# Performance work log

Measured on AMD Instinct MI355X. Metric: run time of the kernel, lower is better.

## Reference

```python
import jax, jax.numpy as jnp
import numpy as np

B, WS, DIM, HEADS, AGENT, PS = 128, 14, 256, 8, 49, 7
N = WS * WS


def conv(x, w, b, pad, groups=1):
    y = jax.lax.conv_general_dilated(x, w, (1, 1), [(pad, pad), (pad, pad)],
                                     dimension_numbers=('NCHW', 'OIHW', 'NCHW'),
                                     feature_group_count=groups)
    return y + b[None, :, None, None]


def bilinear_resize(x, oh, ow):
    # F.interpolate(mode='bilinear', align_corners=False) on last two dims
    ih, iw = x.shape[-2], x.shape[-1]
    def grid(ni, no):
        pos = np.maximum((np.arange(no) + 0.5) * (ni / no) - 0.5, 0.0)
        i0 = np.minimum(np.floor(pos).astype(np.int32), ni - 1)
        i1 = np.minimum(i0 + 1, ni - 1)
        return i0, i1, (pos - i0).astype(np.float32)
    i0h, i1h, lh = grid(ih, oh)
    i0w, i1w, lw = grid(iw, ow)
    xh = x[..., i0h, :] * (1.0 - lh)[:, None] + x[..., i1h, :] * lh[:, None]
    return xh[..., i0w] * (1.0 - lw) + xh[..., i1w] * lw


def rel_pos_index(h, w):
    coords = np.stack(np.meshgrid(np.arange(h), np.arange(w), indexing='ij')).reshape(2, -1)
    rel = (coords[:, :, None] - coords[:, None, :]).transpose(1, 2, 0).copy()
    rel[..., 0] += h - 1
    rel[..., 1] += w - 1
    rel[..., 0] *= 2 * w - 1
    return rel.sum(-1)  # (h*w, h*w)


def cbam(x, caa1_w, caa1_b, caa2_w, caa2_b, cam1_w, cam1_b, cam2_w, cam2_b, sa_w, sa_b):
    # ChannelAttention: both conv stacks act on 1x1 pooled maps -> only kernel centers matter
    avgp = x.mean((2, 3))
    t1 = jax.nn.relu(jnp.einsum('oi,bi->bo', caa1_w[:, :, 1, 1], avgp) + caa1_b)
    y1 = jax.nn.sigmoid(jnp.einsum('oi,bi->bo', caa2_w[:, :, 1, 1], t1) + caa2_b)
    mxp = x.max((2, 3))
    t2 = jax.nn.relu(jnp.einsum('oi,bi->bo', cam1_w[:, :, 0, 0], mxp) + cam1_b)
    y2 = jax.nn.sigmoid(jnp.einsum('oi,bi->bo', cam2_w[:, :, 0, 0], t2) + cam2_b)
    x = jax.nn.sigmoid(y1 + y2)[:, :, None, None] * x
    # Spatial attention
    mask = jnp.concatenate([x.mean(1, keepdims=True), x.max(1, keepdims=True)], axis=1)
    mask = jax.nn.sigmoid(conv(mask, sa_w, sa_b, 4))
    return x * mask


def chan_inter(x, ci1_w, ci1_b, bn_g, bn_b, ci2_w, ci2_b):
    # AdaptiveAvgPool2d(1) then 5x5 convs on 1x1 maps -> kernel-center matmuls; BN in eval mode
    p = x.mean((2, 3))
    t = jnp.einsum('oi,bi->bo', ci1_w[:, :, 2, 2], p) + ci1_b
    t = jax.nn.relu(bn_g * t * (1.0 / np.sqrt(1.0 + 1e-5)) + bn_b)
    return jnp.einsum('oi,bi->bo', ci2_w[:, :, 2, 2], t) + ci2_b


def setup_inputs() -> dict:
    key = jax.random.key(0)
    ks = jax.random.split(key, 40)
    d, r = DIM, DIM // 16
    p = lambda i, shape, s=0.02: jax.random.normal(ks[i], shape, jnp.float32) * s
    return {
        'x': jax.random.normal(ks[0], (B, N, d), jnp.float32),
        'h': WS,
        'w': WS,
        'lka_w': p(1, (3 * d, 1, 5, 5)), 'lka_b': p(2, (3 * d,)),
        'conv5_w': p(3, (d, d, 5, 5)), 'conv5_b': p(4, (d,)),
        'caa1_w': p(5, (r, d, 3, 3)), 'caa1_b': p(6, (r,)),
        'caa2_w': p(7, (d, r, 3, 3)), 'caa2_b': p(8, (d,)),
        'cam1_w': p(9, (r, d, 1, 1)), 'cam1_b': p(10, (r,)),
        'cam2_w': p(11, (d, r, 1, 1)), 'cam2_b': p(12, (d,)),
        'sa_w': p(13, (1, 2, 9, 9)), 'sa_b': p(14, (1,)),
        'ci1_w': p(15, (r, d, 5, 5)), 'ci1_b': p(16, (r,)),
        'bn_g': jnp.ones((r,), jnp.float32), 'bn_b': jnp.zeros((r,), jnp.float32),
        'ci2_w': p(17, (d, r, 5, 5)), 'ci2_b': p(18, (d,)),
        'rpb_table': p(19, ((2 * WS - 1) * (2 * WS - 1), HEADS)),
        'an_bias': p(20, (HEADS, AGENT, 7, 7)), 'na_bias': p(21, (HEADS, AGENT, 7, 7)),
        'ah_bias': p(22, (1, HEADS, AGENT, WS, 1)), 'aw_bias': p(23, (1, HEADS, AGENT, 1, WS)),
        'ha_bias': p(24, (1, HEADS, WS, 1, AGENT)), 'wa_bias': p(25, (1, HEADS, 1, WS, AGENT)),
        'dwc_w': p(26, (d, 1, 5, 5)), 'dwc_b': p(27, (d,)),
        'proj_w': p(28, (d, d)), 'proj_b': p(29, (d,)),
    }


def reference(x, h, w, lka_w, lka_b, conv5_w, conv5_b, caa1_w, caa1_b, caa2_w, caa2_b,
              cam1_w, cam1_b, cam2_w, cam2_b, sa_w, sa_b, ci1_w, ci1_b, bn_g, bn_b,
              ci2_w, ci2_b, rpb_table, an_bias, na_bias, ah_bias, aw_bias, ha_bias,
              wa_bias, dwc_w, dwc_b, proj_w, proj_b):
    b, n, c = x.shape
    heads, agent, ps = HEADS, AGENT, PS
    hd = c // heads
    scale = hd ** (-0.5)

    xc = jnp.transpose(x.reshape(b, h, w, c), (0, 3, 1, 2))  # (b,c,h,w)
    y = conv(xc, lka_w, lka_b, 2, groups=c)                   # depthwise, 3 outputs/group
    k_raw, v_raw, q_raw = y[:, :c], y[:, c:2 * c], y[:, 2 * c:]

    # v branch: conv5 then raw reshape-scramble (faithful to torch .reshape of NCHW), then CBAM
    v5 = jnp.transpose(conv(v_raw, conv5_w, conv5_b, 2).reshape(b, h, w, c), (0, 3, 1, 2))
    vc = cbam(v5, caa1_w, caa1_b, caa2_w, caa2_b, cam1_w, cam1_b, cam2_w, cam2_b, sa_w, sa_b)
    v_feat = jnp.transpose(vc.reshape(b, c, n), (0, 2, 1))    # (b,n,c)

    # adaptive avg/max pool 14->7 == exact 2x2 pooling
    at = q_raw.reshape(b, c, ps, h // ps, ps, w // ps).mean((3, 5)).reshape(b, c, agent).transpose(0, 2, 1)
    atk = k_raw.reshape(b, c, ps, h // ps, ps, w // ps).max((3, 5)).reshape(b, c, agent).transpose(0, 2, 1)

    # raw row-major reshapes of (b,c,h,w) into (b,n,heads,hd): faithful to torch
    q = q_raw.reshape(b, n, heads, hd).transpose(0, 2, 1, 3) * scale
    k = k_raw.reshape(b, n, heads, hd).transpose(0, 2, 1, 3)
    v = v_raw.reshape(b, n, heads, hd).transpose(0, 2, 1, 3)
    v1 = v_feat.reshape(b, n, heads, hd).transpose(0, 2, 1, 3)

    # full window attention with relative position bias
    idx = rel_pos_index(h, w)
    rpb = rpb_table[idx.reshape(-1)].reshape(n, n, heads).transpose(2, 0, 1)
    attn = jax.nn.softmax(jnp.einsum('bhid,bhjd->bhij', q, k) + rpb[None])
    x1 = jnp.einsum('bhij,bhjd->bhid', attn, v).transpose(0, 2, 1, 3).reshape(b, n, c)

    ar = x1.transpose(0, 2, 1).reshape(b, c, h, w)
    cmap = chan_inter(ar, ci1_w, ci1_b, bn_g, bn_b, ci2_w, ci2_b)  # (b,c)
    conv_x2 = jax.nn.sigmoid(cmap)[:, :, None, None] * jnp.transpose(q.reshape(b, h, w, c), (0, 3, 1, 2))

    # agent attention
    at_h = at.reshape(b, agent, heads, hd).transpose(0, 2, 1, 3)
    atk_h = atk.reshape(b, agent, heads, hd).transpose(0, 2, 1, 3)
    pb = bilinear_resize(an_bias, h, w).reshape(1, heads, agent, n) \
         + (ah_bias + aw_bias).reshape(1, heads, agent, n)
    agent_attn = jax.nn.softmax(jnp.einsum('bhad,bhnd->bhan', at_h * scale, k) + pb)
    agent_attn1 = jax.nn.softmax(jnp.einsum('bhad,bhnd->bhan', atk_h * scale, q) + pb)
    agent_v = jnp.einsum('bhan,bhnd->bhad', agent_attn, v1) + jnp.einsum('bhan,bhnd->bhad', agent_attn1, v)

    ab = bilinear_resize(na_bias, h, w).reshape(1, heads, agent, n).transpose(0, 1, 3, 2) \
         + (ha_bias + wa_bias).reshape(1, heads, n, agent)
    q_attn = jax.nn.softmax(jnp.einsum('bhnd,bhad->bhna', q * scale, at_h) + ab)
    k_attn = jax.nn.softmax(jnp.einsum('bhnd,bhad->bhna', k * scale, atk_h) + ab)
    xo = jnp.einsum('bhna,bhad->bhnd', q_attn + k_attn, agent_v).transpose(0, 2, 1, 3).reshape(b, n, c)

    xo = xo + jnp.transpose(conv(conv_x2, dwc_w, dwc_b, 2, groups=c), (0, 2, 3, 1)).reshape(b, n, c)
    qc = jnp.transpose(q.transpose(0, 2, 1, 3).reshape(b, h, w, c), (0, 3, 1, 2))
    xo = xo + jnp.transpose(conv(qc, dwc_w, dwc_b, 2, groups=c), (0, 2, 3, 1)).reshape(b, n, c)

    return xo @ proj_w.T + proj_b
```

## Files before the change

kernel.cpp:

```cpp
#include <hip/hip_runtime.h>

#define NB    128
#define NC    256
#define NPOS  196
#define NHEAD 8
#define NAG   49
#define YSTR  150528
#define VOFF  50176
#define QOFF  100352
#define SCL   0.17677669529663687f

#define WS_Y    0u
#define WS_V5   19267584u
#define WS_AT   25690112u
#define WS_ATK  27295744u
#define WS_CHG  28901376u
#define WS_CMAP 28934144u
#define WS_PBT  28966912u
#define WS_AB   29043744u
#define WS_X1S  29120576u
#define WS_AGV  29153344u
#define WS_XO   30758976u
#define WS_WT   37181504u
#define WS_CWT  37247040u

typedef __attribute__((ext_vector_type(8))) _Float16 half8;
typedef __attribute__((ext_vector_type(8))) short short8;
typedef __attribute__((ext_vector_type(4))) short short4v;
typedef __attribute__((ext_vector_type(4))) float f32x4;
typedef unsigned short ushort_t;
typedef unsigned int uint_t;

__device__ __forceinline__ float sigmoidf_(float x){ return 1.0f/(1.0f+__expf(-x)); }

__device__ __forceinline__ ushort_t f2h(float x){
  _Float16 h = (_Float16)x; return __builtin_bit_cast(ushort_t, h);
}
__device__ __forceinline__ float h2f(ushort_t u){
  return (float)__builtin_bit_cast(_Float16, u);
}

__device__ __forceinline__ float bilin7(const float* __restrict__ src, int i, int j){
  float pi = fmaxf(0.5f*(float)i - 0.25f, 0.f);
  int i0 = (int)pi; if (i0 > 6) i0 = 6;
  int i1 = i0 + 1;  if (i1 > 6) i1 = 6;
  float li = pi - (float)i0;
  float pj = fmaxf(0.5f*(float)j - 0.25f, 0.f);
  int j0 = (int)pj; if (j0 > 6) j0 = 6;
  int j1 = j0 + 1;  if (j1 > 6) j1 = 6;
  float lj = pj - (float)j0;
  float v00 = src[i0*7+j0], v01 = src[i0*7+j1];
  float v10 = src[i1*7+j0], v11 = src[i1*7+j1];
  float t0 = v00*(1.f-lj) + v01*lj;
  float t1 = v10*(1.f-lj) + v11*lj;
  return t0*(1.f-li) + t1*li;
}

__device__ __forceinline__ void conv5x5_row(const float* __restrict__ plane, int r,
                                            const float* __restrict__ w25, float* acc14){
  #pragma unroll
  for (int di = 0; di < 5; ++di){
    const float4* pr = (const float4*)(plane + (r+di)*20);
    float4 p0 = pr[0], p1 = pr[1], p2 = pr[2], p3 = pr[3], p4 = pr[4];
    float row[20] = {p0.x,p0.y,p0.z,p0.w, p1.x,p1.y,p1.z,p1.w, p2.x,p2.y,p2.z,p2.w,
                     p3.x,p3.y,p3.z,p3.w, p4.x,p4.y,p4.z,p4.w};
    #pragma unroll
    for (int dj = 0; dj < 5; ++dj){
      float w = w25[di*5+dj];
      #pragma unroll
      for (int j = 0; j < 14; ++j) acc14[j] = fmaf(row[j+dj], w, acc14[j]);
    }
  }
}

__global__ void k_pbab(const float* __restrict__ an, const float* __restrict__ ah,
                       const float* __restrict__ aw, const float* __restrict__ na,
                       const float* __restrict__ ha, const float* __restrict__ wa,
                       float* __restrict__ PBT, float* __restrict__ AB){
  int bid = blockIdx.x;
  int which = (bid >= 301);
  int t = (which ? bid - 301 : bid)*256 + threadIdx.x;
  if (t >= NHEAD*NPOS*NAG) return;
  int a = t % NAG;
  int r = t / NAG;
  int n = r % NPOS;
  int h = r / NPOS;
  int i = n/14, j = n - (n/14)*14;
  if (!which){
    float v = bilin7(an + ((size_t)h*NAG + a)*49, i, j);
    v += ah[((size_t)h*NAG + a)*14 + i] + aw[((size_t)h*NAG + a)*14 + j];
    PBT[t] = v;
  } else {
    float v = bilin7(na + ((size_t)h*NAG + a)*49, i, j);
    v += ha[((size_t)h*14 + i)*NAG + a] + wa[((size_t)h*14 + j)*NAG + a];
    AB[t] = v;
  }
}

__global__ void k_wprep(const float* __restrict__ cw, ushort_t* __restrict__ Wh,
                        const float* __restrict__ pw, float* __restrict__ WT){
  int bid = blockIdx.x;
  if (bid < 800){
    int base = (bid*256 + threadIdx.x)*8;
    int r   = base >> 8;
    int co  = r & 255;
    int tap = r >> 8;
    int ci0 = base & 255;
    const float* srcb = cw + (size_t)co*6400 + (size_t)ci0*25 + tap;
    short8 o;
    #pragma unroll
    for (int e = 0; e < 8; ++e) o[e] = (short)f2h(srcb[e*25]);
    *(short8*)(Wh + base) = o;
  } else {
    int t = (bid - 800)*256 + threadIdx.x;
    int k = t >> 8, c = t & 255;
    WT[t] = pw[c*256 + k];
  }
}

__global__ __launch_bounds__(256) void k_lka(const float* __restrict__ x, const float* __restrict__ lw,
                                             const float* __restrict__ lb, float* __restrict__ Y){
  int b = blockIdx.x >> 3, gb = blockIdx.x & 7;
  int g0 = gb*32;
  __shared__ __align__(16) float pl[32*360];
  int tid = threadIdx.x;
  for (int t = tid; t < 32*360; t += 256) pl[t] = 0.f;
  __syncthreads();
  for (int t = tid; t < 32*196; t += 256){
    int gl = t & 31, s = t >> 5;
    int i = s/14, j = s - i*14;
    pl[gl*360 + (i+2)*20 + j + 2] = x[((size_t)b*196 + s)*256 + g0 + gl];
  }
  __syncthreads();
  for (int t = tid; t < 96*14; t += 256){
    int ocl = t/14, r = t - ocl*14;
    int o  = g0*3 + ocl;
    int gl = ocl/3;
    float w25[25];
    #pragma unroll
    for (int u = 0; u < 25; ++u) w25[u] = lw[o*25 + u];
    float acc[14];
    float bv = lb[o];
    #pragma unroll
    for (int j = 0; j < 14; ++j) acc[j] = bv;
    conv5x5_row(&pl[gl*360], r, w25, acc);
    float* dst = Y + ((size_t)b*768 + o)*196 + r*14;
    #pragma unroll
    for (int j = 0; j < 14; ++j) dst[j] = acc[j];
  }
}

__global__ __launch_bounds__(256, 2) void k_conv5(const float* __restrict__ Y,
    const ushort_t* __restrict__ Wh, const float* __restrict__ cb, float* __restrict__ V5){
  int b = blockIdx.x >> 2, cog = blockIdx.x & 3;
  int co0 = cog*64;
  __shared__ __align__(16) ushort_t Pt[360*40];
  __shared__ __align__(16) ushort_t Wsm[2*5*64*40];
  float* T = (float*)Wsm;
  int tid  = threadIdx.x;
  int lane = tid & 63, wv = tid >> 6;
  int mrow = lane & 15, quad = lane >> 4;

  for (int t = tid; t < 7200; t += 256) ((uint_t*)Pt)[t] = 0;

  int prow[4];
  #pragma unroll
  for (int mt = 0; mt < 4; ++mt){
    int s = wv*64 + mt*16 + mrow;
    int p0 = 0;
    if (s < 196){ int i = s/14, j = s - i*14; p0 = i*20 + j; }
    prow[mt] = p0;
  }

  f32x4 acc[4][4];
  #pragma unroll
  for (int mt = 0; mt < 4; ++mt)
    #pragma unroll
    for (int nt = 0; nt < 4; ++nt) acc[mt][nt] = (f32x4){0.f,0.f,0.f,0.f};

  const float* src = Y + (size_t)b*YSTR + VOFF;
  int wco = tid >> 2, wpart = tid & 3;
  const ushort_t* wbase = Wh + ((size_t)(co0 + wco))*256 + wpart*8;

  short8 wreg[5];
  #pragma unroll
  for (int tp = 0; tp < 5; ++tp)
    wreg[tp] = *(const short8*)(wbase + (size_t)tp*65536);

  #pragma unroll 1
  for (int cc = 0; cc < 8; ++cc){
    __syncthreads();
    for (int t = tid; t < 784; t += 256){
      int pos = t >> 2, ch = t & 3;
      int i = pos/14, j = pos - i*14;
      int p = (i+2)*20 + j + 2;
      const float* s0 = src + (size_t)(cc*32 + ch*8)*196 + pos;
      short8 pk;
      #pragma unroll
      for (int e = 0; e < 4; ++e){
        float v0 = s0[(2*e)*196];
        float v1 = s0[(2*e+1)*196];
        pk[2*e]   = (short)f2h(v0);
        pk[2*e+1] = (short)f2h(v1);
      }
      *(short8*)&Pt[p*40 + ch*8] = pk;
    }
    #pragma unroll 1
    for (int di = 0; di < 5; ++di){
      int u = cc*5 + di;
      ushort_t* wbuf = Wsm + (u & 1)*12800;
      #pragma unroll
      for (int tp = 0; tp < 5; ++tp)
        *(short8*)&wbuf[(tp*64 + wco)*40 + wpart*8] = wreg[tp];
      if (u < 39){
        int di1 = di + 1, cc1 = cc;
        if (di1 == 5){ di1 = 0; ++cc1; }
        #pragma unroll
        for (int tp = 0; tp < 5; ++tp)
          wreg[tp] = *(const short8*)(wbase + (size_t)(di1*5 + tp)*65536 + cc1*32);
      }
      __syncthreads();
      #pragma unroll
      for (int dj = 0; dj < 5; ++dj){
        half8 a[4], bb[4];
        #pragma unroll
        for (int nt = 0; nt < 4; ++nt){
          int co = nt*16 + mrow;
          bb[nt] = *(const half8*)&wbuf[(dj*64 + co)*40 + quad*8];
        }
        #pragma unroll
        for (int mt = 0; mt < 4; ++mt){
          int p = prow[mt] + di*20 + dj;
          a[mt] = *(const half8*)&Pt[p*40 + quad*8];
        }
        #pragma unroll
        for (int mt = 0; mt < 4; ++mt)
          #pragma unroll
          for (int nt = 0; nt < 4; ++nt)
            acc[mt][nt] = __builtin_amdgcn_mfma_f32_16x16x32_f16(a[mt], bb[nt], acc[mt][nt], 0, 0, 0);
      }
    }
  }

  #pragma unroll
  for (int hf = 0; hf < 2; ++hf){
    __syncthreads();
    #pragma unroll
    for (int ntl = 0; ntl < 2; ++ntl){
      int nt = hf*2 + ntl;
      int col = ntl*16 + mrow;
      #pragma unroll
      for (int mt = 0; mt < 4; ++mt){
        int sbase = wv*64 + mt*16 + quad*4;
        #pragma unroll
        for (int r = 0; r < 4; ++r){
          int s = sbase + r;
          if (s < 196) T[col*200 + s] = acc[mt][nt][r];
        }
      }
    }
    __syncthreads();
    for (int t = tid; t < 6272; t += 256){
      int cl = t / 196;
      int f = (co0 + hf*32)*196 + t;
      float val = T[t + cl*4] + cb[co0 + hf*32 + cl];
      V5[(size_t)b*50176 + (size_t)(f & 255)*196 + (f >> 8)] = val;
    }
  }
}

__global__ __launch_bounds__(256) void k_pool(const float* __restrict__ Y, float* __restrict__ AT, float* __restrict__ ATK){
  int b = blockIdx.x >> 1, half = blockIdx.x & 1;
  int c = (threadIdx.x & 127) + half*128;
  int a0 = (threadIdx.x >> 7) ? 25 : 0;
  int a1 = (threadIdx.x >> 7) ? 49 : 25;
  const float* qp = Y + ((size_t)b*768 + 512 + c)*196;
  const float* kp = Y + ((size_t)b*768 + c)*196;
  for (int a = a0; a < a1; ++a){
    int p1 = a/7, p2 = a - p1*7;
    int s = p1*28 + p2*2;
    float q0 = qp[s], q1 = qp[s+1], q2 = qp[s+14], q3 = qp[s+15];
    AT[((size_t)b*49 + a)*256 + c] = 0.25f*(q0+q1+q2+q3);
    float k0 = kp[s], k1 = kp[s+1], k2 = kp[s+14], k3 = kp[s+15];
    ATK[((size_t)b*49 + a)*256 + c] = fmaxf(fmaxf(k0,k1), fmaxf(k2,k3));
  }
}

__global__ __launch_bounds__(256) void k_cbam(float* __restrict__ V5,
    const float* __restrict__ caa1w, const float* __restrict__ caa1b,
    const float* __restrict__ caa2w, const float* __restrict__ caa2b,
    const float* __restrict__ cam1w, const float* __restrict__ cam1b,
    const float* __restrict__ cam2w, const float* __restrict__ cam2b,
    const float* __restrict__ saw, const float* __restrict__ sab){
  int b = blockIdx.x;
  __shared__ float avg[256], mx[256], t1[16], t2[16], chg[256];
  __shared__ float mp[22*22], xp[22*22];
  __shared__ float mk[196];
  int tid = threadIdx.x, wv = tid >> 6, lane = tid & 63;
  float* v5b = V5 + (size_t)b*50176;

  for (int t = tid; t < 484; t += 256){ mp[t] = 0.f; xp[t] = 0.f; }

  for (int c = wv; c < 256; c += 4){
    float s, m;
    if (lane < 49){
      float4 v = *(const float4*)(v5b + c*196 + lane*4);
      s = v.x + v.y + v.z + v.w;
      m = fmaxf(fmaxf(v.x, v.y), fmaxf(v.z, v.w));
    } else { s = 0.f; m = -1e30f; }
    #pragma unroll
    for (int off = 1; off < 64; off <<= 1){
      s += __shfl_xor(s, off);
      m = fmaxf(m, __shfl_xor(m, off));
    }
    if (lane == 0){ avg[c] = s*(1.0f/196.0f); mx[c] = m; }
  }
  __syncthreads();

  if (tid < 16){
    float a1 = caa1b[tid], a2 = cam1b[tid];
    #pragma unroll 4
    for (int k = 0; k < 256; ++k){
      a1 = fmaf(caa1w[(tid*256 + k)*9 + 4], avg[k], a1);
      a2 = fmaf(cam1w[tid*256 + k], mx[k], a2);
    }
    t1[tid] = fmaxf(a1, 0.f);
    t2[tid] = fmaxf(a2, 0.f);
  }
  __syncthreads();
  {
    float y1 = caa2b[tid], y2 = cam2b[tid];
    #pragma unroll
    for (int k = 0; k < 16; ++k){
      y1 = fmaf(caa2w[(tid*16 + k)*9 + 4], t1[k], y1);
      y2 = fmaf(cam2w[tid*16 + k], t2[k], y2);
    }
    chg[tid] = sigmoidf_(sigmoidf_(y1) + sigmoidf_(y2));
  }
  __syncthreads();

  if (tid < 196){
    int i = tid/14, j = tid - i*14;
    float s = 0.f, m = -1e30f;
    const float* vb = v5b + tid;
    for (int c = 0; c < 256; ++c){
      float v = chg[c] * vb[c*196];
      s += v; m = fmaxf(m, v);
    }
    mp[(i+4)*22 + j+4] = s*(1.f/256.f);
    xp[(i+4)*22 + j+4] = m;
  }
  __syncthreads();
  if (tid < 196){
    int i = tid/14, j = tid - i*14;
    float acc = sab[0];
    for (int di = 0; di < 9; ++di){
      #pragma unroll
      for (int dj = 0; dj < 9; ++dj){
        acc = fmaf(mp[(i+di)*22 + j+dj], saw[di*9+dj], acc);
        acc = fmaf(xp[(i+di)*22 + j+dj], saw[81 + di*9+dj], acc);
      }
    }
    mk[tid] = sigmoidf_(acc);
  }
  __syncthreads();
  if (tid < 196){
    float m = mk[tid];
    float* vb = v5b + tid;
    for (int c = 0; c < 256; ++c) vb[c*196] = chg[c]*vb[c*196]*m;
  }
}

__global__ __launch_bounds__(512, 4) void k_attn3(const float* __restrict__ Y,
    const float* __restrict__ rpbt, float* __restrict__ X1S){
  int b = blockIdx.x >> 3, h = blockIdx.x & 7;
  __shared__ __align__(16) ushort_t Qh[208*32];
  __shared__ __align__(16) ushort_t Kh[208*32];
  __shared__ __align__(16) ushort_t E[80*208];
  __shared__ float rp[736];
  __shared__ int   rpo[208];
  __shared__ float pl2[80][2];
  __shared__ float invl[80];
  __shared__ float wj[208];
  __shared__ float wpart[8][208];
  __shared__ float xpart[16][32];
  int tid = threadIdx.x, wv = tid >> 6, lane = tid & 63;
  int mrow = lane & 15, quad = lane >> 4;
  int sw8 = ((quad ^ ((mrow >> 1) & 3)) << 3);
  const float* yb = Y + (size_t)b*YSTR;

  for (int t = tid; t < 736; t += 512) rp[t] = (t < 729) ? rpbt[t*8 + h] : 0.f;
  for (int j = tid; j < 208; j += 512){
    int jc = (j < 196) ? j : 195;
    int rj = jc/14;
    rpo[j] = rj*27 + (jc - rj*14);
    wj[j] = 0.f;
  }
  for (int t = tid; t < 384; t += 512){
    int arr = t >= 192; int u = t - arr*192;
    ((uint_t*)(arr ? Kh : Qh))[3136 + u] = 0;
  }
  for (int t = tid; t < 3136; t += 512){
    int n = t >> 4, w = t & 15;
    int ws = (((w >> 2) ^ ((n >> 1) & 3)) << 2) | (w & 3);
    const float2 qv = *(const float2*)(yb + QOFF + (size_t)n*256 + h*32 + (w << 1));
    ((uint_t*)Qh)[n*16 + ws] = (uint_t)f2h(qv.x*SCL) | ((uint_t)f2h(qv.y*SCL) << 16);
    const float2 kv = *(const float2*)(yb + (size_t)n*256 + h*32 + (w << 1));
    ((uint_t*)Kh)[n*16 + ws] = (uint_t)f2h(kv.x) | ((uint_t)f2h(kv.y) << 16);
  }
  __syncthreads();

  int mt0 = (wv & 1) ? 7 : 0;
  int mt1 = (wv & 1) ? 13 : 7;

  #pragma unroll 1
  for (int seg = 0; seg < 3; ++seg){
    int base = (seg == 0) ? 0 : (seg == 1) ? 80 : 144;
    int ntl  = (seg == 0) ? 5 : 4;
    int segrows = ntl*16;
    int vrows = 196 - base; if (vrows > segrows) vrows = segrows;

    #pragma unroll 1
    for (int ncl = (wv >> 1); ncl < ntl; ncl += 4){
      int n = base + ncl*16 + mrow;
      half8 bfr = *(const half8*)&Qh[n*32 + sw8];
      int nclamp = (n < 196) ? n : 195;
      int rin = nclamp/14, cin = nclamp - rin*14;
      int bidxn = (rin + 13)*27 + (cin + 13);
      float lsum = 0.f;
      #pragma unroll 1
      for (int mt = mt0; mt < mt1; ++mt){
        half8 afr = *(const half8*)&Kh[(mt*16 + mrow)*32 + sw8];
        f32x4 c = (f32x4){0.f,0.f,0.f,0.f};
        c = __builtin_amdgcn_mfma_f32_16x16x32_f16(afr, bfr, c, 0, 0, 0);
        int j0 = mt*16 + quad*4;
        int4 ro = *(const int4*)&rpo[j0];
        short4v pk;
        #pragma unroll
        for (int r = 0; r < 4; ++r){
          int j = j0 + r;
          int roff = (r == 0) ? ro.x : (r == 1) ? ro.y : (r == 2) ? ro.z : ro.w;
          float e = (j < 196) ? __expf(c[r] + rp[bidxn - roff]) : 0.f;
          lsum += e;
          pk[r] = (short)f2h(e);
        }
        if (n < 196) *(short4v*)&E[(n - base)*208 + j0] = pk;
      }
      lsum += __shfl_xor(lsum, 16);
      lsum += __shfl_xor(lsum, 32);
      if (quad == 0) pl2[n - base][wv & 1] = lsum;
    }
    __syncthreads();
    for (int t = tid; t < vrows; t += 512) invl[t] = 1.f/(pl2[t][0] + pl2[t][1]);
    __syncthreads();

    {
      int j0 = lane*4;
      if (j0 < 208){
        float a0=0.f,a1=0.f,a2=0.f,a3=0.f;
        #pragma unroll 1
        for (int nl = wv; nl < vrows; nl += 8){
          float iv = invl[nl];
          short4v ev = *(const short4v*)&E[nl*208 + j0];
          a0 = fmaf(h2f((ushort_t)ev[0]), iv, a0);
          a1 = fmaf(h2f((ushort_t)ev[1]), iv, a1);
          a2 = fmaf(h2f((ushort_t)ev[2]), iv, a2);
          a3 = fmaf(h2f((ushort_t)ev[3]), iv, a3);
        }
        *(f32x4*)&wpart[wv][j0] = (f32x4){a0,a1,a2,a3};
      }
    }
    __syncthreads();
    for (int j = tid; j < 208; j += 512){
      float s = wj[j];
      #pragma unroll
      for (int g = 0; g < 8; ++g) s += wpart[g][j];
      wj[j] = s;
    }
    __syncthreads();
  }

  {
    int d = tid & 31, g = tid >> 5;
    float s = 0.f;
    #pragma unroll 1
    for (int u = 0; u < 13; ++u){
      int j = g*13 + u;
      s = fmaf(wj[j], yb[VOFF + (size_t)j*256 + h*32 + d], s);
    }
    xpart[g][d] = s;
  }
  __syncthreads();
  if (tid < 32){
    float s = 0.f;
    #pragma unroll
    for (int g2 = 0; g2 < 16; ++g2) s += xpart[g2][tid];
    X1S[(size_t)b*256 + h*32 + tid] = s*(1.f/196.f);
  }
}

__global__ __launch_bounds__(256) void k_cinter(const float* __restrict__ X1S,
    const float* __restrict__ ci1w, const float* __restrict__ ci1b,
    const float* __restrict__ bng, const float* __restrict__ bnb,
    const float* __restrict__ ci2w, const float* __restrict__ ci2b, float* __restrict__ CMAP){
  int b = blockIdx.x, c = threadIdx.x;
  __shared__ float p[256], tt[16];
  p[c] = X1S[b*256 + c];
  __syncthreads();
  if (c < 16){
    float a = ci1b[c];
    #pragma unroll 4
    for (int k = 0; k < 256; ++k) a = fmaf(ci1w[(c*256+k)*25 + 12], p[k], a);
    const float invs = 0.9999950000375f;
    tt[c] = fmaxf(fmaf(bng[c]*invs, a, bnb[c]), 0.f);
  }
  __syncthreads();
  float a = ci2b[c];
  #pragma unroll
  for (int k = 0; k < 16; ++k) a = fmaf(ci2w[(c*16+k)*25 + 12], tt[k], a);
  CMAP[b*256 + c] = sigmoidf_(a);
}

__global__ __launch_bounds__(256) void k_agentv(const float* __restrict__ Y, const float* __restrict__ V5,
    const float* __restrict__ AT, const float* __restrict__ ATK,
    const float* __restrict__ PBT, float* __restrict__ AGV){
  int b = blockIdx.x >> 3, h = blockIdx.x & 7;
  __shared__ __align__(16) ushort_t ST[64*232];
  __shared__ __align__(16) ushort_t R[8704];
  __shared__ float psum[4*64];
  __shared__ float inv0s[64], inv1s[64];
  int tid = threadIdx.x, wv = tid >> 6, lane = tid & 63;
  int mrow = lane & 15, quad = lane >> 4;
  int sw8 = ((quad ^ ((mrow >> 1) & 3)) << 3);
  const float* yb = Y + (size_t)b*YSTR;
  ushort_t* Kh = R;
  ushort_t* Ah = R + 6656;
  ushort_t* Vt = R;
  f32x4 out0[2], out1[2];

  for (int t = tid; t < 512; t += 256){
    int a = t >> 3, c2 = 208 + ((t & 7) << 1);
    *(uint_t*)&ST[a*232 + c2] = 0;
  }

  #pragma unroll 1
  for (int pass = 0; pass < 2; ++pass){
    for (int t = tid; t < 192; t += 256) ((uint_t*)Kh)[3136 + t] = 0;
    for (int t = tid; t < 240; t += 256) ((uint_t*)Ah)[784 + t] = 0;
    {
      const float* rsrc = yb + (pass ? QOFF : 0) + h*32;
      for (int t = tid; t < 3136; t += 256){
        int n = t >> 4, w = t & 15;
        const float2 v = *(const float2*)(rsrc + (size_t)n*256 + (w << 1));
        int ws = (((w >> 2) ^ ((n >> 1) & 3)) << 2) | (w & 3);
        ((uint_t*)Kh)[n*16 + ws] = (uint_t)f2h(v.x) | ((uint_t)f2h(v.y) << 16);
      }
      const float* asrc = (pass ? ATK : AT) + (size_t)b*49*256 + h*32;
      for (int t = tid; t < 784; t += 256){
        int a = t >> 4, w = t & 15;
        const float2 v = *(const float2*)(asrc + (size_t)a*256 + (w << 1));
        int ws = (((w >> 2) ^ ((a >> 1) & 3)) << 2) | (w & 3);
        ((uint_t*)Ah)[a*16 + ws] = (uint_t)f2h(v.x) | ((uint_t)f2h(v.y) << 16);
      }
    }
    __syncthreads();
    {
      float lscl = pass ? 0.03125f : SCL;
      int ag = wv*16 + mrow;
      half8 bfr = *(const half8*)&Ah[ag*32 + sw8];
      #pragma unroll 1
      for (int mt = 0; mt < 13; ++mt){
        half8 afr = *(const half8*)&Kh[(mt*16 + mrow)*32 + sw8];
        f32x4 c = (f32x4){0.f,0.f,0.f,0.f};
        c = __builtin_amdgcn_mfma_f32_16x16x32_f16(afr, bfr, c, 0, 0, 0);
        int n0 = mt*16 + quad*4;
        short4v pk;
        #pragma unroll
        for (int r = 0; r < 4; ++r){
          int n = n0 + r;
          float pb = PBT[((size_t)h*196 + n)*49 + ag];
          float e = (n < 196) ? __expf(fmaf(c[r], lscl, pb)) : 0.f;
          pk[r] = (short)f2h(e);
        }
        *(short4v*)&ST[ag*232 + n0] = pk;
      }
    }
    __syncthreads();
    {
      int a = tid >> 2, q = tid & 3;
      float s = 0.f;
      #pragma unroll
      for (int u = 0; u < 7; ++u){
        short8 v8 = *(const short8*)&ST[a*232 + q*56 + u*8];
        #pragma unroll
        for (int e = 0; e < 8; ++e) s += h2f((ushort_t)v8[e]);
      }
      psum[q*64 + a] = s;
    }
    if (pass == 0){
      const float* vsrc = V5 + (size_t)b*50176 + h*32*196;
      for (int t = tid; t < 3136; t += 256){
        int d = t / 98, np = t - (t/98)*98;
        const float2 v = *(const float2*)(vsrc + (size_t)d*196 + 2*np);
        *(uint_t*)&Vt[d*232 + 2*np] = (uint_t)f2h(v.x) | ((uint_t)f2h(v.y) << 16);
      }
    } else {
      const float* vsrc = yb + VOFF + h*32;
      for (int t = tid; t < 3136; t += 256){
        int np = t >> 4, dp = t & 15;
        const float2 v = *(const float2*)(vsrc + (size_t)np*256 + (dp << 1));
        Vt[(2*dp)*232 + np]     = f2h(v.x);
        Vt[(2*dp + 1)*232 + np] = f2h(v.y);
      }
    }
    for (int t = tid; t < 448; t += 256){
      int d = t / 14, c2 = 196 + 2*(t - (t/14)*14);
      *(uint_t*)&Vt[d*232 + c2] = 0;
    }
    __syncthreads();
    {
      f32x4* outp = pass ? out1 : out0;
      #pragma unroll
      for (int nt = 0; nt < 2; ++nt){
        f32x4 c = (f32x4){0.f,0.f,0.f,0.f};
        #pragma unroll
        for (int ks = 0; ks < 7; ++ks){
          half8 afr = *(const half8*)&ST[(wv*16 + mrow)*232 + ks*32 + quad*8];
          half8 bfr = *(const half8*)&Vt[(nt*16 + mrow)*232 + ks*32 + quad*8];
          c = __builtin_amdgcn_mfma_f32_16x16x32_f16(afr, bfr, c, 0, 0, 0);
        }
        outp[nt] = c;
      }
      if (tid < 64){
        float s = psum[tid] + psum[64+tid] + psum[128+tid] + psum[192+tid];
        float* invp = pass ? inv1s : inv0s;
        invp[tid] = 1.f / s;
      }
    }
    __syncthreads();
  }
  #pragma unroll
  for (int nt = 0; nt < 2; ++nt){
    int d = nt*16 + mrow;
    #pragma unroll
    for (int r = 0; r < 4; ++r){
      int a = wv*16 + quad*4 + r;
      if (a < 49)
        AGV[(((size_t)(b*8 + h)*49) + a)*32 + d] = out0[nt][r]*inv0s[a] + out1[nt][r]*inv1s[a];
    }
  }
}

__global__ __launch_bounds__(256) void k_xo1(const float* __restrict__ Y,
    const float* __restrict__ AT, const float* __restrict__ ATK,
    const float* __restrict__ AB, const float* __restrict__ AGV, float* __restrict__ XO){
  int b = blockIdx.x >> 3, h = blockIdx.x & 7;
  __shared__ __align__(16) ushort_t ST[208*72];
  __shared__ __align__(16) ushort_t Kh[208*32];
  __shared__ __align__(16) ushort_t Ah[64*32];
  __shared__ __align__(16) ushort_t AGVt[32*64];
  __shared__ float invs[208];
  int tid = threadIdx.x, wv = tid >> 6, lane = tid & 63;
  int mrow = lane & 15, quad = lane >> 4;
  int sw8 = ((quad ^ ((mrow >> 1) & 3)) << 3);
  const float* yb = Y + (size_t)b*YSTR;
  f32x4 acc[4][2];
  #pragma unroll
  for (int i = 0; i < 4; ++i){
    acc[i][0] = (f32x4){0.f,0.f,0.f,0.f};
    acc[i][1] = (f32x4){0.f,0.f,0.f,0.f};
  }

  for (int t = tid; t < 1664; t += 256){
    int rw = t >> 3, c2 = 48 + ((t & 7) << 1);
    *(uint_t*)&ST[rw*72 + c2] = 0;
  }
  {
    const float* agvb = AGV + (size_t)(b*8 + h)*49*32;
    for (int t = tid; t < 2048; t += 256){
      int d = t >> 6, a = t & 63;
      int as = ((((a >> 3) ^ (d & 7)) & 7) << 3) | (a & 7);
      AGVt[d*64 + as] = (a < 49) ? f2h(agvb[a*32 + d]) : (ushort_t)0;
    }
  }

  #pragma unroll 1
  for (int pass = 0; pass < 2; ++pass){
    {
      const float* rsrc = yb + (pass ? 0 : QOFF) + h*32;
      for (int t = tid; t < 3136; t += 256){
        int n = t >> 4, w = t & 15;
        const float2 v = *(const float2*)(rsrc + (size_t)n*256 + (w << 1));
        int ws = (((w >> 2) ^ ((n >> 1) & 3)) << 2) | (w & 3);
        ((uint_t*)Kh)[n*16 + ws] = (uint_t)f2h(v.x) | ((uint_t)f2h(v.y) << 16);
      }
      const float* asrc = (pass ? ATK : AT) + (size_t)b*49*256 + h*32;
      for (int t = tid; t < 784; t += 256){
        int a = t >> 4, w = t & 15;
        const float2 v = *(const float2*)(asrc + (size_t)a*256 + (w << 1));
        int ws = (((w >> 2) ^ ((a >> 1) & 3)) << 2) | (w & 3);
        ((uint_t*)Ah)[a*16 + ws] = (uint_t)f2h(v.x) | ((uint_t)f2h(v.y) << 16);
      }
    }
    __syncthreads();
    {
      float lscl = pass ? SCL : 0.03125f;
      int ag = wv*16 + mrow;
      half8 bfr = *(const half8*)&Ah[ag*32 + sw8];
      #pragma unroll 1
      for (int mt = 0; mt < 13; ++mt){
        half8 afr = *(const half8*)&Kh[(mt*16 + mrow)*32 + sw8];
        f32x4 c = (f32x4){0.f,0.f,0.f,0.f};
        c = __builtin_amdgcn_mfma_f32_16x16x32_f16(afr, bfr, c, 0, 0, 0);
        #pragma unroll
        for (int r = 0; r < 4; ++r){
          int n = mt*16 + quad*4 + r;
          if (n < 196 && ag < 49){
            float e = __expf(fmaf(c[r], lscl, AB[((size_t)h*196 + n)*49 + ag]));
            ST[n*72 + ag] = f2h(e);
          }
        }
      }
    }
    __syncthreads();
    if (tid < 196){
      float s = 0.f;
      #pragma unroll
      for (int u = 0; u < 7; ++u){
        short8 v8 = *(const short8*)&ST[tid*72 + u*8];
        #pragma unroll
        for (int e = 0; e < 8; ++e) s += h2f((ushort_t)v8[e]);
      }
      invs[tid] = 1.f / s;
    }
    __syncthreads();
    {
      int i = 0;
      #pragma unroll 1
      for (int mt = wv; mt < 13; mt += 4, ++i){
        #pragma unroll
        for (int nt = 0; nt < 2; ++nt){
          f32x4 c = (f32x4){0.f,0.f,0.f,0.f};
          #pragma unroll
          for (int ks = 0; ks < 2; ++ks){
            half8 afr = *(const half8*)&ST[(mt*16 + mrow)*72 + ks*32 + quad*8];
            half8 bfr = *(const half8*)&AGVt[(nt*16 + mrow)*64 + ((((ks*4 + quad) ^ (mrow & 7)) & 7) << 3)];
            c = __builtin_amdgcn_mfma_f32_16x16x32_f16(afr, bfr, c, 0, 0, 0);
          }
          #pragma unroll
          for (int r = 0; r < 4; ++r){
            int n = mt*16 + quad*4 + r;
            if (n < 196) acc[i][nt][r] = fmaf(c[r], invs[n], acc[i][nt][r]);
          }
        }
      }
    }
    __syncthreads();
  }
  {
    int i = 0;
    #pragma unroll 1
    for (int mt = wv; mt < 13; mt += 4, ++i){
      #pragma unroll
      for (int nt = 0; nt < 2; ++nt){
        #pragma unroll
        for (int r = 0; r < 4; ++r){
          int n = mt*16 + quad*4 + r;
          if (n < 196)
            XO[((size_t)b*196 + n)*256 + h*32 + nt*16 + mrow] = acc[i][nt][r];
        }
      }
    }
  }
}

__global__ __launch_bounds__(256) void k_dwc(const float* __restrict__ Y, const float* __restrict__ CMAP,
    const float* __restrict__ dw, const float* __restrict__ db, float* __restrict__ XO){
  int b = blockIdx.x >> 3, cg = blockIdx.x & 7;
  int c0 = cg*32;
  __shared__ __align__(16) float pl[32*360];
  int tid = threadIdx.x;
  for (int t = tid; t < 32*360; t += 256) pl[t] = 0.f;
  __syncthreads();
  const float* yq = Y + (size_t)b*YSTR + QOFF;
  for (int t = tid; t < 32*196; t += 256){
    int cl = t & 31, s = t >> 5;
    int c = c0 + cl;
    int G = s*256 + c;
    int hh = G / 6272;
    int rem = G - hh*6272;
    int n = rem >> 5, d = rem & 31;
    float cx2 = CMAP[b*256 + c] * yq[n*256 + hh*32 + d];
    float qc  = yq[G];
    float v = SCL*(cx2 + qc);
    int i = s/14, j = s - i*14;
    pl[cl*360 + (i+2)*20 + j + 2] = v;
  }
  __syncthreads();
  for (int t = tid; t < 32*14; t += 256){
    int cl = t/14, r = t - cl*14;
    int c = c0 + cl;
    float w25[25];
    #pragma unroll
    for (int u = 0; u < 25; ++u) w25[u] = dw[c*25 + u];
    float acc[14];
    float b2 = 2.f*db[c];
    #pragma unroll
    for (int j = 0; j < 14; ++j) acc[j] = b2;
    conv5x5_row(&pl[cl*360], r, w25, acc);
    float* dst = XO + ((size_t)b*196 + r*14)*256 + c;
    #pragma unroll
    for (int j = 0; j < 14; ++j) dst[j*256] += acc[j];
  }
}

__global__ __launch_bounds__(256) void k_proj(const float* __restrict__ XO, const float* __restrict__ WT,
    const float* __restrict__ pbias, float* __restrict__ OUT){
  int bb = blockIdx.x / 7, nt = blockIdx.x % 7;
  int n0 = nt*28;
  int c = threadIdx.x;
  const float* xb = XO + ((size_t)bb*196 + n0)*256;
  float acc[28];
  #pragma unroll
  for (int r = 0; r < 28; ++r) acc[r] = 0.f;
  for (int k = 0; k < 256; k += 4){
    float w0 = WT[(k+0)*256 + c];
    float w1 = WT[(k+1)*256 + c];
    float w2 = WT[(k+2)*256 + c];
    float w3 = WT[(k+3)*256 + c];
    #pragma unroll
    for (int r = 0; r < 28; ++r){
      float4 xv = *(const float4*)(xb + r*256 + k);
      acc[r] = fmaf(xv.x, w0, fmaf(xv.y, w1, fmaf(xv.z, w2, fmaf(xv.w, w3, acc[r]))));
    }
  }
  float bv = pbias[c];
  float* dst = OUT + ((size_t)bb*196 + n0)*256 + c;
  #pragma unroll
  for (int r = 0; r < 28; ++r) dst[r*256] = acc[r] + bv;
}

extern "C" void kernel_launch(void* const* d_in, const int* in_sizes, int n_in,
                              void* d_out, int out_size, void* d_ws, size_t ws_size,
                              hipStream_t stream){
  (void)in_sizes; (void)n_in; (void)out_size; (void)ws_size;
  const float* x       = (const float*)d_in[0];
  const float* lka_w   = (const float*)d_in[3];
  const float* lka_b   = (const float*)d_in[4];
  const float* conv5_w = (const float*)d_in[5];
  const float* conv5_b = (const float*)d_in[6];
  const float* caa1_w  = (const float*)d_in[7];
  const float* caa1_b  = (const float*)d_in[8];
  const float* caa2_w  = (const float*)d_in[9];
  const float* caa2_b  = (const float*)d_in[10];
  const float* cam1_w  = (const float*)d_in[11];
  const float* cam1_b  = (const float*)d_in[12];
  const float* cam2_w  = (const float*)d_in[13];
  const float* cam2_b  = (const float*)d_in[14];
  const float* sa_w    = (const float*)d_in[15];
  const float* sa_b    = (const float*)d_in[16];
  const float* ci1_w   = (const float*)d_in[17];
  const float* ci1_b   = (const float*)d_in[18];
  const float* bn_g    = (const float*)d_in[19];
  const float* bn_b    = (const float*)d_in[20];
  const float* ci2_w   = (const float*)d_in[21];
  const float* ci2_b   = (const float*)d_in[22];
  const float* rpbt    = (const float*)d_in[23];
  const float* an_bias = (const float*)d_in[24];
  const float* na_bias = (const float*)d_in[25];
  const float* ah_bias = (const float*)d_in[26];
  const float* aw_bias = (const float*)d_in[27];
  const float* ha_bias = (const float*)d_in[28];
  const float* wa_bias = (const float*)d_in[29];
  const float* dwc_w   = (const float*)d_in[30];
  const float* dwc_b   = (const float*)d_in[31];
  const float* proj_w  = (const float*)d_in[32];
  const float* proj_b  = (const float*)d_in[33];
  float* out = (float*)d_out;
  float* ws = (float*)d_ws;

  float* Y    = ws + WS_Y;
  float* V5   = ws + WS_V5;
  float* AT   = ws + WS_AT;
  float* ATK  = ws + WS_ATK;
  float* CMAP = ws + WS_CMAP;
  float* PBT  = ws + WS_PBT;
  float* AB   = ws + WS_AB;
  float* X1S  = ws + WS_X1S;
  float* AGV  = ws + WS_AGV;
  float* XO   = ws + WS_XO;
  float* WT   = ws + WS_WT;
  ushort_t* Wh = (ushort_t*)(ws + WS_CWT);

  k_pbab <<<602, 256, 0, stream>>>(an_bias, ah_bias, aw_bias, na_bias, ha_bias, wa_bias, PBT, AB);
  k_wprep<<<1056, 256, 0, stream>>>(conv5_w, Wh, proj_w, WT);
  k_lka  <<<1024, 256, 0, stream>>>(x, lka_w, lka_b, Y);
  k_conv5<<<512, 256, 0, stream>>>(Y, Wh, conv5_b, V5);
  k_pool <<<256, 256, 0, stream>>>(Y, AT, ATK);
  k_cbam <<<128, 256, 0, stream>>>(V5, caa1_w, caa1_b, caa2_w, caa2_b,
                                   cam1_w, cam1_b, cam2_w, cam2_b, sa_w, sa_b);
  k_attn3<<<1024, 512, 0, stream>>>(Y, rpbt, X1S);
  k_cinter<<<128, 256, 0, stream>>>(X1S, ci1_w, ci1_b, bn_g, bn_b, ci2_w, ci2_b, CMAP);
  k_agentv<<<1024, 256, 0, stream>>>(Y, V5, AT, ATK, PBT, AGV);
  k_xo1  <<<1024, 256, 0, stream>>>(Y, AT, ATK, AB, AGV, XO);
  k_dwc  <<<1024, 256, 0, stream>>>(Y, CMAP, dwc_w, dwc_b, XO);
  k_proj <<<896, 256, 0, stream>>>(XO, WT, proj_b, out);
}
```

Before: 794.9 us.

## Split CBAM into parallel pooling and gate kernels, fold scaling into agentv

The single 128-block CBAM kernel is split in two. A 1024-block kernel computes the per-channel avg and max pools, and a second kernel computes the channel gate and spatial mask, summing the channel-weighted maps with two thread halves. The final in-place rescale of V5 is removed. The channel gate and spatial mask are applied on the fly when k_agentv loads V5. This aims to cut the low-occupancy serial pass over V5 and one full read-write of it, at the cost of an extra launch and small workspace buffers for MX and MK.

New measurement: 732.0 us (median of 2 runs). 7.9% less time.

```diff
diff --git a/kernel.cpp b/kernel.cpp
--- a/kernel.cpp
+++ b/kernel.cpp
@@ -23,6 +23,8 @@
 #define WS_XO   30758976u
 #define WS_WT   37181504u
 #define WS_CWT  37247040u
+#define WS_MX   38066240u
+#define WS_MK   38099008u
 
 typedef __attribute__((ext_vector_type(8))) _Float16 half8;
 typedef __attribute__((ext_vector_type(8))) short short8;
@@ -286,22 +288,14 @@
   }
 }
 
-__global__ __launch_bounds__(256) void k_cbam(float* __restrict__ V5,
-    const float* __restrict__ caa1w, const float* __restrict__ caa1b,
-    const float* __restrict__ caa2w, const float* __restrict__ caa2b,
-    const float* __restrict__ cam1w, const float* __restrict__ cam1b,
-    const float* __restrict__ cam2w, const float* __restrict__ cam2b,
-    const float* __restrict__ saw, const float* __restrict__ sab){
-  int b = blockIdx.x;
-  __shared__ float avg[256], mx[256], t1[16], t2[16], chg[256];
-  __shared__ float mp[22*22], xp[22*22];
-  __shared__ float mk[196];
+__global__ __launch_bounds__(256) void k_cbam_a2(const float* __restrict__ V5,
+    float* __restrict__ AVG, float* __restrict__ MX){
+  int b = blockIdx.x >> 3, oct = blockIdx.x & 7;
   int tid = threadIdx.x, wv = tid >> 6, lane = tid & 63;
-  float* v5b = V5 + (size_t)b*50176;
-
-  for (int t = tid; t < 484; t += 256){ mp[t] = 0.f; xp[t] = 0.f; }
-
-  for (int c = wv; c < 256; c += 4){
+  const float* v5b = V5 + (size_t)b*50176;
+  #pragma unroll
+  for (int i = 0; i < 8; ++i){
+    int c = oct*32 + i*4 + wv;
     float s, m;
     if (lane < 49){
       float4 v = *(const float4*)(v5b + c*196 + lane*4);
@@ -313,8 +307,29 @@
       s += __shfl_xor(s, off);
       m = fmaxf(m, __shfl_xor(m, off));
     }
-    if (lane == 0){ avg[c] = s*(1.0f/196.0f); mx[c] = m; }
-  }
+    if (lane == 0){
+      AVG[b*256 + c] = s*(1.0f/196.0f);
+      MX[b*256 + c]  = m;
+    }
+  }
+}
+
+__global__ __launch_bounds__(512) void k_cbam_b2(const float* __restrict__ V5,
+    float* __restrict__ AVGCHG, const float* __restrict__ MX,
+    const float* __restrict__ caa1w, const float* __restrict__ caa1b,
+    const float* __restrict__ caa2w, const float* __restrict__ caa2b,
+    const float* __restrict__ cam1w, const float* __restrict__ cam1b,
+    const float* __restrict__ cam2w, const float* __restrict__ cam2b,
+    const float* __restrict__ saw, const float* __restrict__ sab,
+    float* __restrict__ MK){
+  int b = blockIdx.x;
+  __shared__ float avg[256], mx[256], t1[16], t2[16], chg[256];
+  __shared__ float sp[2][196], sx[2][196];
+  __shared__ float mp[22*22], xp[22*22];
+  int tid = threadIdx.x;
+  if (tid < 256) avg[tid] = AVGCHG[b*256 + tid];
+  else           mx[tid - 256] = MX[b*256 + tid - 256];
+  for (int t = tid; t < 484; t += 512){ mp[t] = 0.f; xp[t] = 0.f; }
   __syncthreads();
 
   if (tid < 16){
@@ -328,27 +343,36 @@
     t2[tid] = fmaxf(a2, 0.f);
   }
   __syncthreads();
-  {
+  if (tid < 256){
     float y1 = caa2b[tid], y2 = cam2b[tid];
     #pragma unroll
     for (int k = 0; k < 16; ++k){
       y1 = fmaf(caa2w[(tid*16 + k)*9 + 4], t1[k], y1);
       y2 = fmaf(cam2w[tid*16 + k], t2[k], y2);
     }
-    chg[tid] = sigmoidf_(sigmoidf_(y1) + sigmoidf_(y2));
-  }
-  __syncthreads();
-
+    float g = sigmoidf_(sigmoidf_(y1) + sigmoidf_(y2));
+    chg[tid] = g;
+    AVGCHG[b*256 + tid] = g;
+  }
+  __syncthreads();
+
+  {
+    int g = tid >> 8, pos = tid & 255;
+    if (pos < 196){
+      const float* vb = V5 + (size_t)b*50176 + pos;
+      float s = 0.f, m = -1e30f;
+      for (int c = g*128; c < g*128 + 128; ++c){
+        float v = chg[c] * vb[c*196];
+        s += v; m = fmaxf(m, v);
+      }
+      sp[g][pos] = s; sx[g][pos] = m;
+    }
+  }
+  __syncthreads();
   if (tid < 196){
     int i = tid/14, j = tid - i*14;
-    float s = 0.f, m = -1e30f;
-    const float* vb = v5b + tid;
-    for (int c = 0; c < 256; ++c){
-      float v = chg[c] * vb[c*196];
-      s += v; m = fmaxf(m, v);
-    }
-    mp[(i+4)*22 + j+4] = s*(1.f/256.f);
-    xp[(i+4)*22 + j+4] = m;
+    mp[(i+4)*22 + j+4] = (sp[0][tid] + sp[1][tid])*(1.f/256.f);
+    xp[(i+4)*22 + j+4] = fmaxf(sx[0][tid], sx[1][tid]);
   }
   __syncthreads();
   if (tid < 196){
@@ -361,13 +385,7 @@
         acc = fmaf(xp[(i+di)*22 + j+dj], saw[81 + di*9+dj], acc);
       }
     }
-    mk[tid] = sigmoidf_(acc);
-  }
-  __syncthreads();
-  if (tid < 196){
-    float m = mk[tid];
-    float* vb = v5b + tid;
-    for (int c = 0; c < 256; ++c) vb[c*196] = chg[c]*vb[c*196]*m;
+    MK[(size_t)b*196 + tid] = sigmoidf_(acc);
   }
 }
 
@@ -522,6 +540,7 @@
 }
 
 __global__ __launch_bounds__(256) void k_agentv(const float* __restrict__ Y, const float* __restrict__ V5,
+    const float* __restrict__ CHG, const float* __restrict__ MK,
     const float* __restrict__ AT, const float* __restrict__ ATK,
     const float* __restrict__ PBT, float* __restrict__ AGV){
   int b = blockIdx.x >> 3, h = blockIdx.x & 7;
@@ -529,6 +548,8 @@
   __shared__ __align__(16) ushort_t R[8704];
   __shared__ float psum[4*64];
   __shared__ float inv0s[64], inv1s[64];
+  __shared__ float mks[196];
+  __shared__ float chgs[32];
   int tid = threadIdx.x, wv = tid >> 6, lane = tid & 63;
   int mrow = lane & 15, quad = lane >> 4;
   int sw8 = ((quad ^ ((mrow >> 1) & 3)) << 3);
@@ -538,6 +559,8 @@
   ushort_t* Vt = R;
   f32x4 out0[2], out1[2];
 
+  if (tid < 196) mks[tid] = MK[(size_t)b*196 + tid];
+  if (tid >= 224) chgs[tid - 224] = CHG[(size_t)b*256 + h*32 + (tid - 224)];
   for (int t = tid; t < 512; t += 256){
     int a = t >> 3, c2 = 208 + ((t & 7) << 1);
     *(uint_t*)&ST[a*232 + c2] = 0;
@@ -602,7 +625,10 @@
       for (int t = tid; t < 3136; t += 256){
         int d = t / 98, np = t - (t/98)*98;
         const float2 v = *(const float2*)(vsrc + (size_t)d*196 + 2*np);
-        *(uint_t*)&Vt[d*232 + 2*np] = (uint_t)f2h(v.x) | ((uint_t)f2h(v.y) << 16);
+        float g = chgs[d];
+        float a0 = (g*v.x)*mks[2*np];
+        float a1 = (g*v.y)*mks[2*np + 1];
+        *(uint_t*)&Vt[d*232 + 2*np] = (uint_t)f2h(a0) | ((uint_t)f2h(a1) << 16);
       }
     } else {
       const float* vsrc = yb + VOFF + h*32;
@@ -883,6 +909,7 @@
   float* V5   = ws + WS_V5;
   float* AT   = ws + WS_AT;
   float* ATK  = ws + WS_ATK;
+  float* CHG  = ws + WS_CHG;
   float* CMAP = ws + WS_CMAP;
   float* PBT  = ws + WS_PBT;
   float* AB   = ws + WS_AB;
@@ -891,17 +918,20 @@
   float* XO   = ws + WS_XO;
   float* WT   = ws + WS_WT;
   ushort_t* Wh = (ushort_t*)(ws + WS_CWT);
+  float* MXp  = ws + WS_MX;
+  float* MKp  = ws + WS_MK;
 
   k_pbab <<<602, 256, 0, stream>>>(an_bias, ah_bias, aw_bias, na_bias, ha_bias, wa_bias, PBT, AB);
   k_wprep<<<1056, 256, 0, stream>>>(conv5_w, Wh, proj_w, WT);
   k_lka  <<<1024, 256, 0, stream>>>(x, lka_w, lka_b, Y);
   k_conv5<<<512, 256, 0, stream>>>(Y, Wh, conv5_b, V5);
   k_pool <<<256, 256, 0, stream>>>(Y, AT, ATK);
-  k_cbam <<<128, 256, 0, stream>>>(V5, caa1_w, caa1_b, caa2_w, caa2_b,
-                                   cam1_w, cam1_b, cam2_w, cam2_b, sa_w, sa_b);
+  k_cbam_a2<<<1024, 256, 0, stream>>>(V5, CHG, MXp);
+  k_cbam_b2<<<128, 512, 0, stream>>>(V5, CHG, MXp, caa1_w, caa1_b, caa2_w, caa2_b,
+                                     cam1_w, cam1_b, cam2_w, cam2_b, sa_w, sa_b, MKp);
   k_attn3<<<1024, 512, 0, stream>>>(Y, rpbt, X1S);
   k_cinter<<<128, 256, 0, stream>>>(X1S, ci1_w, ci1_b, bn_g, bn_b, ci2_w, ci2_b, CMAP);
-  k_agentv<<<1024, 256, 0, stream>>>(Y, V5, AT, ATK, PBT, AGV);
+  k_agentv<<<1024, 256, 0, stream>>>(Y, V5, CHG, MKp, AT, ATK, PBT, AGV);
   k_xo1  <<<1024, 256, 0, stream>>>(Y, AT, ATK, AB, AGV, XO);
   k_dwc  <<<1024, 256, 0, stream>>>(Y, CMAP, dwc_w, dwc_b, XO);
   k_proj <<<896, 256, 0, stream>>>(XO, WT, proj_b, out);
```
